# Kernel optimization log

Measured on AMD Instinct MI355X. Metric: run time of the kernel, lower is better.

## Reference

```python
import jax, jax.numpy as jnp
import numpy as np

B, S, E = 2, 2048, 1024
NH, NKV = 16, 4
HD = E // NH
GS = NH // NKV


def setup_inputs() -> dict:
    key = jax.random.key(0)
    ks = jax.random.split(key, 8)
    sc = 0.02
    query = jax.random.normal(ks[0], (B, S, E), dtype=jnp.float32)
    key_t = jax.random.normal(ks[1], (B, S, E), dtype=jnp.float32)
    value = jax.random.normal(ks[2], (B, S, E), dtype=jnp.float32)
    # causal mask, broadcast shape [1,1,S,S] as in source (unsqueeze(0).unsqueeze(0))
    attn_mask = jnp.tril(jnp.ones((S, S), dtype=bool))[None, None]
    Wq = jax.random.normal(ks[3], (NH * HD, E), dtype=jnp.float32) * sc
    Wk = jax.random.normal(ks[4], (NKV * HD, E), dtype=jnp.float32) * sc
    Wv = jax.random.normal(ks[5], (NKV * HD, E), dtype=jnp.float32) * sc
    Wo = jax.random.normal(ks[6], (E, NH * HD), dtype=jnp.float32) * sc
    return {"query": query, "key": key_t, "value": value, "attn_mask": attn_mask,
            "Wq": Wq, "Wk": Wk, "Wv": Wv, "Wo": Wo}


def reference(query, key, value, attn_mask, Wq, Wk, Wv, Wo):
    # projections (nn.Linear, bias=False: y = x @ W.T)
    q = (query @ Wq.T).reshape(B, S, NH, HD).transpose(0, 2, 1, 3)   # [B,NH,S,HD]
    k = (key @ Wk.T).reshape(B, S, NKV, HD).transpose(0, 2, 1, 3)    # [B,NKV,S,HD]
    v = (value @ Wv.T).reshape(B, S, NKV, HD).transpose(0, 2, 1, 3)  # [B,NKV,S,HD]
    # repeat_interleave over head dim to match query heads
    k = jnp.repeat(k, GS, axis=1)  # [B,NH,S,HD]
    v = jnp.repeat(v, GS, axis=1)
    scale = 1.0 / np.sqrt(HD).astype(np.float32)
    scores = jnp.einsum('bhqd,bhkd->bhqk', q, k) * scale  # [B,NH,S,S]
    scores = jnp.where(attn_mask, scores, -jnp.inf)
    weights = jax.nn.softmax(scores, axis=-1)
    out = jnp.einsum('bhqk,bhkd->bhqd', weights, v)        # [B,NH,S,HD]
    out = out.transpose(0, 2, 1, 3).reshape(B, S, NH * HD)
    return out @ Wo.T  # [B,S,E]
```

## Files before the change

### kernel.cpp

```cpp
#include <hip/hip_runtime.h>
#include <hip/hip_bf16.h>

typedef __attribute__((ext_vector_type(8))) short bf16x8;
typedef __attribute__((ext_vector_type(4))) float f32x4;

#define MFMA16(a, b, c) __builtin_amdgcn_mfma_f32_16x16x32_bf16((a), (b), (c), 0, 0, 0)
#define ASYNC16(g, l)                                                     \
    __builtin_amdgcn_global_load_lds(                                     \
        (const __attribute__((address_space(1))) void*)(g),               \
        (__attribute__((address_space(3))) void*)(l), 16, 0, 0)

constexpr int B_ = 2, S_ = 2048, E_ = 1024, NH_ = 16, NKV_ = 4, HD_ = 64;

__global__ __launch_bounds__(256) void cvt_all(
    const float* __restrict__ s0, const float* __restrict__ s1,
    const float* __restrict__ s2, const float* __restrict__ s3,
    const float* __restrict__ s4, const float* __restrict__ s5,
    const float* __restrict__ s6,
    __hip_bfloat16* __restrict__ d0, __hip_bfloat16* __restrict__ d1,
    __hip_bfloat16* __restrict__ d2, __hip_bfloat16* __restrict__ d3,
    __hip_bfloat16* __restrict__ d4, __hip_bfloat16* __restrict__ d5,
    __hip_bfloat16* __restrict__ d6)
{
    int id = blockIdx.x;
    const float* s;
    __hip_bfloat16* d;
    if (id < 6144) {
        const int which = id >> 11;
        s = which == 0 ? s0 : (which == 1 ? s1 : s2);
        d = which == 0 ? d0 : (which == 1 ? d1 : d2);
        id &= 2047;
    } else if (id < 6656) { s = s3; d = d3; id -= 6144; }
    else if (id < 7168)   { s = s4; d = d4; id -= 6656; }
    else if (id < 7296)   { s = s5; d = d5; id -= 7168; }
    else                  { s = s6; d = d6; id -= 7296; }

    const size_t i = ((size_t)id * 256 + threadIdx.x) * 8;
    const float4 f0 = *reinterpret_cast<const float4*>(s + i);
    const float4 f1 = *reinterpret_cast<const float4*>(s + i + 4);
    union { __hip_bfloat16 h[8]; uint4 u; } t;
    t.h[0] = __float2bfloat16(f0.x); t.h[1] = __float2bfloat16(f0.y);
    t.h[2] = __float2bfloat16(f0.z); t.h[3] = __float2bfloat16(f0.w);
    t.h[4] = __float2bfloat16(f1.x); t.h[5] = __float2bfloat16(f1.y);
    t.h[6] = __float2bfloat16(f1.z); t.h[7] = __float2bfloat16(f1.w);
    *reinterpret_cast<uint4*>(d + i) = t.u;
}

__device__ __forceinline__ void gemm_core(
    const __hip_bfloat16* __restrict__ A,
    const __hip_bfloat16* __restrict__ W,
    void* __restrict__ C,
    const int N, const int mode, const int m0, const int n0,
    __hip_bfloat16* sA, __hip_bfloat16* sW)
{
    const int tid  = threadIdx.x;
    const int l    = tid & 63;
    const int w    = tid >> 6;
    const int quad = l >> 4;
    const int lan  = l & 15;
    const int wm   = (w >> 1) * 32;
    const int wn   = (w & 1) * 64;

    const int srow  = w * 8 + (l >> 3);
    const int scolL = (l & 7) * 8;
    const int scolG = ((l & 7) ^ (l >> 3)) * 8;

    f32x4 acc[2][4] = {};

#define STAGE(buf, kb)                                                    \
    {                                                                     \
        _Pragma("unroll")                                                 \
        for (int q = 0; q < 2; ++q) {                                     \
            const int r_ = q * 32 + srow;                                 \
            ASYNC16(A + (size_t)(m0 + r_) * E_ + (kb) + scolG,            \
                    sA + (buf) * 4096 + r_ * 64 + scolL);                 \
        }                                                                 \
        _Pragma("unroll")                                                 \
        for (int q = 0; q < 4; ++q) {                                     \
            const int r_ = q * 32 + srow;                                 \
            ASYNC16(W + (size_t)(n0 + r_) * E_ + (kb) + scolG,            \
                    sW + (buf) * 8192 + r_ * 64 + scolL);                 \
        }                                                                 \
    }

    STAGE(0, 0)
    int cur = 0;
#pragma unroll 1
    for (int t = 0; t < 16; ++t) {
        __syncthreads();
        if (t < 15) STAGE(cur ^ 1, (t + 1) * 64)

#pragma unroll
        for (int kk = 0; kk < 2; ++kk) {
            bf16x8 af[2], bf[4];
            const int ca = ((kk * 4 + quad) ^ (lan & 7)) * 8;
#pragma unroll
            for (int i = 0; i < 2; ++i)
                af[i] = *reinterpret_cast<const bf16x8*>(
                    sA + cur * 4096 + (wm + i * 16 + lan) * 64 + ca);
#pragma unroll
            for (int j = 0; j < 4; ++j)
                bf[j] = *reinterpret_cast<const bf16x8*>(
                    sW + cur * 8192 + (wn + j * 16 + lan) * 64 + ca);
#pragma unroll
            for (int i = 0; i < 2; ++i)
#pragma unroll
                for (int j = 0; j < 4; ++j)
                    acc[i][j] = MFMA16(af[i], bf[j], acc[i][j]);
        }
        cur ^= 1;
    }
#undef STAGE

#pragma unroll
    for (int i = 0; i < 2; ++i)
#pragma unroll
        for (int j = 0; j < 4; ++j)
#pragma unroll
            for (int r = 0; r < 4; ++r) {
                const int gm = m0 + wm + i * 16 + quad * 4 + r;
                const int gn = n0 + wn + j * 16 + lan;
                const float v = acc[i][j][r];
                if (mode == 2) {
                    ((float*)C)[(size_t)gm * N + gn] = v;
                } else {
                    const __hip_bfloat16 hv = __float2bfloat16(v);
                    if (mode == 0)
                        ((__hip_bfloat16*)C)[(size_t)gm * N + gn] = hv;
                    else
                        ((__hip_bfloat16*)C)
                            [((size_t)(gm >> 11) * N + gn) * (size_t)S_ +
                             (gm & 2047)] = hv;
                }
            }
}

__global__ __launch_bounds__(256) void gemm_qkv(
    const __hip_bfloat16* __restrict__ qb, const __hip_bfloat16* __restrict__ kb,
    const __hip_bfloat16* __restrict__ vb, const __hip_bfloat16* __restrict__ Wqb,
    const __hip_bfloat16* __restrict__ Wkb, const __hip_bfloat16* __restrict__ Wvb,
    __hip_bfloat16* __restrict__ QO, __hip_bfloat16* __restrict__ Kws,
    __hip_bfloat16* __restrict__ VT)
{
    __shared__ __hip_bfloat16 sA[2 * 4096];
    __shared__ __hip_bfloat16 sW[2 * 8192];
    int id = blockIdx.x;
    const __hip_bfloat16 *A, *W;
    void* C;
    int N, mode, bx, by;
    if (id < 512)      { A = qb; W = Wqb; C = QO;  N = 1024; mode = 0; bx = id & 7; by = id >> 3; }
    else if (id < 640) { id -= 512; A = kb; W = Wkb; C = Kws; N = 256; mode = 0; bx = id & 1; by = id >> 1; }
    else               { id -= 640; A = vb; W = Wvb; C = VT;  N = 256; mode = 1; bx = id & 1; by = id >> 1; }
    gemm_core(A, W, C, N, mode, by * 64, bx * 128, sA, sW);
}

__global__ __launch_bounds__(256) void gemm_out(
    const __hip_bfloat16* __restrict__ QO, const __hip_bfloat16* __restrict__ Wob,
    float* __restrict__ out)
{
    __shared__ __hip_bfloat16 sA[2 * 4096];
    __shared__ __hip_bfloat16 sW[2 * 8192];
    const int id = blockIdx.x;
    gemm_core(QO, Wob, out, 1024, 2, (id >> 3) * 64, (id & 7) * 128, sA, sW);
}

__global__ __launch_bounds__(256) void attn(
    __hip_bfloat16* QO,
    const __hip_bfloat16* __restrict__ Kp,
    const __hip_bfloat16* __restrict__ VT)
{
    __shared__ __hip_bfloat16 sK[64][64];
    __shared__ __hip_bfloat16 sV[64][64];

    const int bx   = blockIdx.x;
    const int h    = blockIdx.y;
    const int b    = blockIdx.z;
    const int hk   = h >> 2;
    const int tid  = threadIdx.x;
    const int l    = tid & 63;
    const int w    = tid >> 6;
    const int quad = l >> 4;
    const int lan  = l & 15;
    const bool hi  = quad >= 2;
    const float KSC = 0.125f * 1.44269504088896340736f;

    const int idxA = (((quad & 1) * 32) + lan) * 4;
    const int idxB = idxA + 64;

    const int kr  = tid >> 2;
    const int s0c = (tid & 3) * 2;
    const int sw0 = (s0c ^ (kr & 7)) * 8;
    const int sw1 = ((s0c + 1) ^ (kr & 7)) * 8;
    const int kc  = s0c * 8;

    const int swq0 = (quad ^ (lan & 7)) * 8;
    const int swq1 = ((4 + quad) ^ (lan & 7)) * 8;

    const __hip_bfloat16* kg =
        Kp + ((size_t)((b * S_ + kr) * NKV_) + hk) * HD_ + kc;
    const __hip_bfloat16* vg =
        VT + ((size_t)((b * NKV_ + hk) * HD_) + kr) * S_ + kc;
    const size_t kstride = (size_t)64 * NKV_ * HD_;

    for (int half = 0; half < 2; ++half) {
        const int qt  = half ? (31 - bx) : bx;
        const int qr0 = qt * 64 + w * 16;
        const int qme = qr0 + lan;

        const __hip_bfloat16* qp =
            QO + ((size_t)((b * S_ + qme) * NH_) + h) * HD_ + quad * 8;
        const bf16x8 aq0 = *reinterpret_cast<const bf16x8*>(qp);
        const bf16x8 aq1 = *reinterpret_cast<const bf16x8*>(qp + 32);

        float m_i = -3.0e38f, l_i = 0.f;
        f32x4 acc_o[4] = {};

        uint4 kv0 = *reinterpret_cast<const uint4*>(kg);
        uint4 kv1 = *reinterpret_cast<const uint4*>(kg + 8);
        uint4 vv0 = *reinterpret_cast<const uint4*>(vg);
        uint4 vv1 = *reinterpret_cast<const uint4*>(vg + 8);

        for (int kt = 0; kt <= qt; ++kt) {
            __syncthreads();
            *reinterpret_cast<uint4*>(&sK[kr][sw0]) = kv0;
            *reinterpret_cast<uint4*>(&sK[kr][sw1]) = kv1;
            *reinterpret_cast<uint4*>(&sV[kr][sw0]) = vv0;
            *reinterpret_cast<uint4*>(&sV[kr][sw1]) = vv1;
            __syncthreads();

            if (kt < qt) {
                const __hip_bfloat16* kn = kg + (size_t)(kt + 1) * kstride;
                const __hip_bfloat16* vn = vg + (size_t)(kt + 1) * 64;
                kv0 = *reinterpret_cast<const uint4*>(kn);
                kv1 = *reinterpret_cast<const uint4*>(kn + 8);
                vv0 = *reinterpret_cast<const uint4*>(vn);
                vv1 = *reinterpret_cast<const uint4*>(vn + 8);
            }

            f32x4 accs[4] = {};
#pragma unroll
            for (int j = 0; j < 4; ++j) {
                bf16x8 bk0 = *reinterpret_cast<const bf16x8*>(&sK[j * 16 + lan][swq0]);
                accs[j] = MFMA16(bk0, aq0, accs[j]);
                bf16x8 bk1 = *reinterpret_cast<const bf16x8*>(&sK[j * 16 + lan][swq1]);
                accs[j] = MFMA16(bk1, aq1, accs[j]);
            }

            if (kt == qt) {
#pragma unroll
                for (int j = 0; j < 4; ++j)
#pragma unroll
                    for (int r = 0; r < 4; ++r) {
                        const int kcg = kt * 64 + j * 16 + quad * 4 + r;
                        if (kcg > qme) accs[j][r] = -1e30f;
                    }
            }

            float tm = accs[0][0];
#pragma unroll
            for (int j = 0; j < 4; ++j)
#pragma unroll
                for (int r = 0; r < 4; ++r) tm = fmaxf(tm, accs[j][r]);
            tm = fmaxf(tm, __shfl_xor(tm, 16));
            tm = fmaxf(tm, __shfl_xor(tm, 32));

            if (__any((tm - m_i) * KSC > 8.0f)) {
                const float mnew  = fmaxf(m_i, tm);
                const float alpha = exp2f((m_i - mnew) * KSC);
                l_i *= alpha;
                m_i  = mnew;
#pragma unroll
                for (int dd = 0; dd < 4; ++dd)
#pragma unroll
                    for (int r = 0; r < 4; ++r) acc_o[dd][r] *= alpha;
            }

            float ps = 0.f;
#pragma unroll
            for (int j = 0; j < 4; ++j)
#pragma unroll
                for (int r = 0; r < 4; ++r) {
                    const float p = exp2f((accs[j][r] - m_i) * KSC);
                    accs[j][r] = p;
                    ps += p;
                }
            ps += __shfl_xor(ps, 16);
            ps += __shfl_xor(ps, 32);
            l_i += ps;

            uint pk[4][2];
#pragma unroll
            for (int j = 0; j < 4; ++j)
#pragma unroll
                for (int hh = 0; hh < 2; ++hh) {
                    union { __hip_bfloat16 bh[2]; uint u; } t;
                    t.bh[0] = __float2bfloat16(accs[j][2 * hh]);
                    t.bh[1] = __float2bfloat16(accs[j][2 * hh + 1]);
                    pk[j][hh] = t.u;
                }

#pragma unroll
            for (int kk = 0; kk < 2; ++kk) {
                union { uint u[4]; bf16x8 v; } pb;
#pragma unroll
                for (int w2 = 0; w2 < 4; ++w2) {
                    const int idx = (w2 & 2) ? idxB : idxA;
                    const uint a = (uint)__builtin_amdgcn_ds_bpermute(
                        idx, (int)pk[2 * kk][w2 & 1]);
                    const uint bb = (uint)__builtin_amdgcn_ds_bpermute(
                        idx, (int)pk[2 * kk + 1][w2 & 1]);
                    pb.u[w2] = hi ? bb : a;
                }
#pragma unroll
                for (int dd = 0; dd < 4; ++dd) {
                    const int swv = ((kk * 4 + quad) ^ (lan & 7)) * 8;
                    bf16x8 av = *reinterpret_cast<const bf16x8*>(
                        &sV[dd * 16 + lan][swv]);
                    acc_o[dd] = MFMA16(av, pb.v, acc_o[dd]);
                }
            }
        }

        const float inv = 1.0f / l_i;
        __hip_bfloat16* op =
            QO + ((size_t)((b * S_ + qme) * NH_) + h) * HD_ + quad * 4;
#pragma unroll
        for (int dd = 0; dd < 4; ++dd) {
            union { __hip_bfloat16 bh[4]; uint2 u; } t;
#pragma unroll
            for (int r = 0; r < 4; ++r)
                t.bh[r] = __float2bfloat16(acc_o[dd][r] * inv);
            *reinterpret_cast<uint2*>(op + dd * 16) = t.u;
        }
    }
}

extern "C" void kernel_launch(void* const* d_in, const int* in_sizes, int n_in,
                              void* d_out, int out_size, void* d_ws, size_t ws_size,
                              hipStream_t stream) {
    const float* q  = (const float*)d_in[0];
    const float* k  = (const float*)d_in[1];
    const float* v  = (const float*)d_in[2];
    const float* Wq = (const float*)d_in[4];
    const float* Wk = (const float*)d_in[5];
    const float* Wv = (const float*)d_in[6];
    const float* Wo = (const float*)d_in[7];

    __hip_bfloat16* ws = (__hip_bfloat16*)d_ws;
    __hip_bfloat16* qb   = ws;
    __hip_bfloat16* kb   = qb  + 4194304;
    __hip_bfloat16* vb   = kb  + 4194304;
    __hip_bfloat16* QO   = vb  + 4194304;
    __hip_bfloat16* Kws  = QO  + 4194304;
    __hip_bfloat16* VT   = Kws + 1048576;
    __hip_bfloat16* Wqb  = VT  + 1048576;
    __hip_bfloat16* Wob  = Wqb + 1048576;
    __hip_bfloat16* Wkb  = Wob + 1048576;
    __hip_bfloat16* Wvb  = Wkb + 262144;

    cvt_all<<<dim3(7424), 256, 0, stream>>>(
        q, k, v, Wq, Wo, Wk, Wv, qb, kb, vb, Wqb, Wob, Wkb, Wvb);

    gemm_qkv<<<dim3(768), 256, 0, stream>>>(
        qb, kb, vb, Wqb, Wkb, Wvb, QO, Kws, VT);

    attn<<<dim3(16, NH_, B_), 256, 0, stream>>>(QO, Kws, VT);

    gemm_out<<<dim3(512), 256, 0, stream>>>(QO, Wob, (float*)d_out);
}
```

Measured before the change: 210.7 us.

## Use triple-buffered LDS pipeline with partial vmcnt waits in GEMM core

Converts the GEMM core's double-buffered async global-to-LDS loop into a three-stage ring buffer that prefetches two k-tiles ahead. It waits only for the oldest stage via s_waitcnt vmcnt(6) before the barrier, so memory latency overlaps more with MFMA work. This raises LDS usage per block from 48KB to 72KB, which may reduce occupancy for the projection and output GEMMs.

```diff
diff --git a/kernel.cpp b/kernel.cpp
--- a/kernel.cpp
+++ b/kernel.cpp
@@ -83,34 +83,49 @@
         }                                                                 \
     }
 
+#define COMPUTE(buf)                                                      \
+    {                                                                     \
+        _Pragma("unroll")                                                 \
+        for (int kk = 0; kk < 2; ++kk) {                                  \
+            bf16x8 af[2], bf[4];                                          \
+            const int ca = ((kk * 4 + quad) ^ (lan & 7)) * 8;             \
+            _Pragma("unroll")                                             \
+            for (int i = 0; i < 2; ++i)                                   \
+                af[i] = *reinterpret_cast<const bf16x8*>(                 \
+                    sA + (buf) * 4096 + (wm + i * 16 + lan) * 64 + ca);   \
+            _Pragma("unroll")                                             \
+            for (int j = 0; j < 4; ++j)                                   \
+                bf[j] = *reinterpret_cast<const bf16x8*>(                 \
+                    sW + (buf) * 8192 + (wn + j * 16 + lan) * 64 + ca);   \
+            _Pragma("unroll")                                             \
+            for (int i = 0; i < 2; ++i)                                   \
+                _Pragma("unroll")                                         \
+                for (int j = 0; j < 4; ++j)                               \
+                    acc[i][j] = MFMA16(af[i], bf[j], acc[i][j]);          \
+        }                                                                 \
+    }
+
     STAGE(0, 0)
+    STAGE(1, 64)
     int cur = 0;
 #pragma unroll 1
-    for (int t = 0; t < 16; ++t) {
-        __syncthreads();
-        if (t < 15) STAGE(cur ^ 1, (t + 1) * 64)
-
-#pragma unroll
-        for (int kk = 0; kk < 2; ++kk) {
-            bf16x8 af[2], bf[4];
-            const int ca = ((kk * 4 + quad) ^ (lan & 7)) * 8;
-#pragma unroll
-            for (int i = 0; i < 2; ++i)
-                af[i] = *reinterpret_cast<const bf16x8*>(
-                    sA + cur * 4096 + (wm + i * 16 + lan) * 64 + ca);
-#pragma unroll
-            for (int j = 0; j < 4; ++j)
-                bf[j] = *reinterpret_cast<const bf16x8*>(
-                    sW + cur * 8192 + (wn + j * 16 + lan) * 64 + ca);
-#pragma unroll
-            for (int i = 0; i < 2; ++i)
-#pragma unroll
-                for (int j = 0; j < 4; ++j)
-                    acc[i][j] = MFMA16(af[i], bf[j], acc[i][j]);
+    for (int t = 0; t < 15; ++t) {
+        __builtin_amdgcn_sched_barrier(0);
+        asm volatile("s_waitcnt vmcnt(6)" ::: "memory");
+        __builtin_amdgcn_s_barrier();
+        if (t < 14) {
+            int nb = cur + 2; if (nb >= 3) nb -= 3;
+            STAGE(nb, (t + 2) * 64)
         }
-        cur ^= 1;
+        COMPUTE(cur)
+        cur = (cur == 2) ? 0 : cur + 1;
     }
+    __builtin_amdgcn_sched_barrier(0);
+    asm volatile("s_waitcnt vmcnt(0)" ::: "memory");
+    __builtin_amdgcn_s_barrier();
+    COMPUTE(cur)
 #undef STAGE
+#undef COMPUTE
 
 #pragma unroll
     for (int i = 0; i < 2; ++i)
@@ -142,8 +157,8 @@
     __hip_bfloat16* __restrict__ QO, __hip_bfloat16* __restrict__ Kws,
     __hip_bfloat16* __restrict__ VT)
 {
-    __shared__ __hip_bfloat16 sA[2 * 4096];
-    __shared__ __hip_bfloat16 sW[2 * 8192];
+    __shared__ __hip_bfloat16 sA[3 * 4096];
+    __shared__ __hip_bfloat16 sW[3 * 8192];
     int id = blockIdx.x;
     const __hip_bfloat16 *A, *W;
     void* C;
@@ -158,8 +173,8 @@
     const __hip_bfloat16* __restrict__ QO, const __hip_bfloat16* __restrict__ Wob,
     float* __restrict__ out)
 {
-    __shared__ __hip_bfloat16 sA[2 * 4096];
-    __shared__ __hip_bfloat16 sW[2 * 8192];
+    __shared__ __hip_bfloat16 sA[3 * 4096];
+    __shared__ __hip_bfloat16 sW[3 * 8192];
     const int id = blockIdx.x;
     gemm_core(QO, Wob, out, 1024, 2, (id >> 3) * 64, (id & 7) * 128, sA, sW);
 }
```

Result: slower. 219.0 us (+3.9%).

## Process 128-row query tiles per block to reuse K/V tiles across two row groups

Applied to the files above, without the earlier changes.

Each wave in the attention kernel now handles two 16-row query groups (32 rows), so a block covers 128 query rows and every K/V tile loaded into shared memory feeds twice as many MFMAs. The grid is halved to 8x16x2 blocks, still with causal pairing of tiles. The aim is to cut LDS/global traffic and sync overhead per unit of work. The cost is more registers (doubled accumulators), fewer blocks for the GPU to schedule, and some wasted work on the diagonal tile, where masking now spans two K tiles.

```diff
diff --git a/kernel.cpp b/kernel.cpp
--- a/kernel.cpp
+++ b/kernel.cpp
@@ -203,24 +203,31 @@
     const size_t kstride = (size_t)64 * NKV_ * HD_;
 
     for (int half = 0; half < 2; ++half) {
-        const int qt  = half ? (31 - bx) : bx;
-        const int qr0 = qt * 64 + w * 16;
-        const int qme = qr0 + lan;
-
-        const __hip_bfloat16* qp =
-            QO + ((size_t)((b * S_ + qme) * NH_) + h) * HD_ + quad * 8;
-        const bf16x8 aq0 = *reinterpret_cast<const bf16x8*>(qp);
-        const bf16x8 aq1 = *reinterpret_cast<const bf16x8*>(qp + 32);
-
-        float m_i = -3.0e38f, l_i = 0.f;
-        f32x4 acc_o[4] = {};
+        const int qt  = half ? (15 - bx) : bx;
+        const int qr0 = qt * 128 + w * 32;
+
+        bf16x8 aq[2][2];
+        int qme[2];
+#pragma unroll
+        for (int g = 0; g < 2; ++g) {
+            qme[g] = qr0 + g * 16 + lan;
+            const __hip_bfloat16* qp =
+                QO + ((size_t)((b * S_ + qme[g]) * NH_) + h) * HD_ + quad * 8;
+            aq[g][0] = *reinterpret_cast<const bf16x8*>(qp);
+            aq[g][1] = *reinterpret_cast<const bf16x8*>(qp + 32);
+        }
+
+        float m_i[2] = {-3.0e38f, -3.0e38f};
+        float l_i[2] = {0.f, 0.f};
+        f32x4 acc_o[2][4] = {};
 
         uint4 kv0 = *reinterpret_cast<const uint4*>(kg);
         uint4 kv1 = *reinterpret_cast<const uint4*>(kg + 8);
         uint4 vv0 = *reinterpret_cast<const uint4*>(vg);
         uint4 vv1 = *reinterpret_cast<const uint4*>(vg + 8);
 
-        for (int kt = 0; kt <= qt; ++kt) {
+        const int ktmax = 2 * qt + 1;
+        for (int kt = 0; kt <= ktmax; ++kt) {
             __syncthreads();
             *reinterpret_cast<uint4*>(&sK[kr][sw0]) = kv0;
             *reinterpret_cast<uint4*>(&sK[kr][sw1]) = kv1;
@@ -228,7 +235,7 @@
             *reinterpret_cast<uint4*>(&sV[kr][sw1]) = vv1;
             __syncthreads();
 
-            if (kt < qt) {
+            if (kt < ktmax) {
                 const __hip_bfloat16* kn = kg + (size_t)(kt + 1) * kstride;
                 const __hip_bfloat16* vn = vg + (size_t)(kt + 1) * 64;
                 kv0 = *reinterpret_cast<const uint4*>(kn);
@@ -237,100 +244,113 @@
                 vv1 = *reinterpret_cast<const uint4*>(vn + 8);
             }
 
-            f32x4 accs[4] = {};
+            f32x4 accs[2][4] = {};
 #pragma unroll
             for (int j = 0; j < 4; ++j) {
                 bf16x8 bk0 = *reinterpret_cast<const bf16x8*>(&sK[j * 16 + lan][swq0]);
-                accs[j] = MFMA16(bk0, aq0, accs[j]);
                 bf16x8 bk1 = *reinterpret_cast<const bf16x8*>(&sK[j * 16 + lan][swq1]);
-                accs[j] = MFMA16(bk1, aq1, accs[j]);
-            }
-
-            if (kt == qt) {
+                accs[0][j] = MFMA16(bk0, aq[0][0], accs[0][j]);
+                accs[0][j] = MFMA16(bk1, aq[0][1], accs[0][j]);
+                accs[1][j] = MFMA16(bk0, aq[1][0], accs[1][j]);
+                accs[1][j] = MFMA16(bk1, aq[1][1], accs[1][j]);
+            }
+
+            if (kt >= 2 * qt) {
+#pragma unroll
+                for (int g = 0; g < 2; ++g)
+#pragma unroll
+                    for (int j = 0; j < 4; ++j)
+#pragma unroll
+                        for (int r = 0; r < 4; ++r) {
+                            const int kcg = kt * 64 + j * 16 + quad * 4 + r;
+                            if (kcg > qme[g]) accs[g][j][r] = -1e30f;
+                        }
+            }
+
+            uint pk[2][4][2];
+#pragma unroll
+            for (int g = 0; g < 2; ++g) {
+                float tm = accs[g][0][0];
 #pragma unroll
                 for (int j = 0; j < 4; ++j)
 #pragma unroll
+                    for (int r = 0; r < 4; ++r) tm = fmaxf(tm, accs[g][j][r]);
+                tm = fmaxf(tm, __shfl_xor(tm, 16));
+                tm = fmaxf(tm, __shfl_xor(tm, 32));
+
+                if (__any((tm - m_i[g]) * KSC > 8.0f)) {
+                    const float mnew  = fmaxf(m_i[g], tm);
+                    const float alpha = exp2f((m_i[g] - mnew) * KSC);
+                    l_i[g] *= alpha;
+                    m_i[g]  = mnew;
+#pragma unroll
+                    for (int dd = 0; dd < 4; ++dd)
+#pragma unroll
+                        for (int r = 0; r < 4; ++r) acc_o[g][dd][r] *= alpha;
+                }
+
+                float ps = 0.f;
+#pragma unroll
+                for (int j = 0; j < 4; ++j)
+#pragma unroll
                     for (int r = 0; r < 4; ++r) {
-                        const int kcg = kt * 64 + j * 16 + quad * 4 + r;
-                        if (kcg > qme) accs[j][r] = -1e30f;
+                        const float p = exp2f((accs[g][j][r] - m_i[g]) * KSC);
+                        accs[g][j][r] = p;
+                        ps += p;
                     }
-            }
-
-            float tm = accs[0][0];
-#pragma unroll
-            for (int j = 0; j < 4; ++j)
-#pragma unroll
-                for (int r = 0; r < 4; ++r) tm = fmaxf(tm, accs[j][r]);
-            tm = fmaxf(tm, __shfl_xor(tm, 16));
-            tm = fmaxf(tm, __shfl_xor(tm, 32));
-
-            if (__any((tm - m_i) * KSC > 8.0f)) {
-                const float mnew  = fmaxf(m_i, tm);
-                const float alpha = exp2f((m_i - mnew) * KSC);
-                l_i *= alpha;
-                m_i  = mnew;
-#pragma unroll
-                for (int dd = 0; dd < 4; ++dd)
-#pragma unroll
-                    for (int r = 0; r < 4; ++r) acc_o[dd][r] *= alpha;
-            }
-
-            float ps = 0.f;
-#pragma unroll
-            for (int j = 0; j < 4; ++j)
-#pragma unroll
-                for (int r = 0; r < 4; ++r) {
-                    const float p = exp2f((accs[j][r] - m_i) * KSC);
-                    accs[j][r] = p;
-                    ps += p;
-                }
-            ps += __shfl_xor(ps, 16);
-            ps += __shfl_xor(ps, 32);
-            l_i += ps;
-
-            uint pk[4][2];
-#pragma unroll
-            for (int j = 0; j < 4; ++j)
-#pragma unroll
-                for (int hh = 0; hh < 2; ++hh) {
-                    union { __hip_bfloat16 bh[2]; uint u; } t;
-                    t.bh[0] = __float2bfloat16(accs[j][2 * hh]);
-                    t.bh[1] = __float2bfloat16(accs[j][2 * hh + 1]);
-                    pk[j][hh] = t.u;
-                }
+                ps += __shfl_xor(ps, 16);
+                ps += __shfl_xor(ps, 32);
+                l_i[g] += ps;
+
+#pragma unroll
+                for (int j = 0; j < 4; ++j)
+#pragma unroll
+                    for (int hh = 0; hh < 2; ++hh) {
+                        union { __hip_bfloat16 bh[2]; uint u; } t;
+                        t.bh[0] = __float2bfloat16(accs[g][j][2 * hh]);
+                        t.bh[1] = __float2bfloat16(accs[g][j][2 * hh + 1]);
+                        pk[g][j][hh] = t.u;
+                    }
+            }
 
 #pragma unroll
             for (int kk = 0; kk < 2; ++kk) {
-                union { uint u[4]; bf16x8 v; } pb;
-#pragma unroll
-                for (int w2 = 0; w2 < 4; ++w2) {
-                    const int idx = (w2 & 2) ? idxB : idxA;
-                    const uint a = (uint)__builtin_amdgcn_ds_bpermute(
-                        idx, (int)pk[2 * kk][w2 & 1]);
-                    const uint bb = (uint)__builtin_amdgcn_ds_bpermute(
-                        idx, (int)pk[2 * kk + 1][w2 & 1]);
-                    pb.u[w2] = hi ? bb : a;
-                }
+                union { uint u[4]; bf16x8 v; } pb[2];
+#pragma unroll
+                for (int g = 0; g < 2; ++g)
+#pragma unroll
+                    for (int w2 = 0; w2 < 4; ++w2) {
+                        const int idx = (w2 & 2) ? idxB : idxA;
+                        const uint a = (uint)__builtin_amdgcn_ds_bpermute(
+                            idx, (int)pk[g][2 * kk][w2 & 1]);
+                        const uint bb = (uint)__builtin_amdgcn_ds_bpermute(
+                            idx, (int)pk[g][2 * kk + 1][w2 & 1]);
+                        pb[g].u[w2] = hi ? bb : a;
+                    }
 #pragma unroll
                 for (int dd = 0; dd < 4; ++dd) {
                     const int swv = ((kk * 4 + quad) ^ (lan & 7)) * 8;
                     bf16x8 av = *reinterpret_cast<const bf16x8*>(
                         &sV[dd * 16 + lan][swv]);
-                    acc_o[dd] = MFMA16(av, pb.v, acc_o[dd]);
+                    acc_o[0][dd] = MFMA16(av, pb[0].v, acc_o[0][dd]);
+                    acc_o[1][dd] = MFMA16(av, pb[1].v, acc_o[1][dd]);
                 }
             }
         }
 
-        const float inv = 1.0f / l_i;
-        __hip_bfloat16* op =
-            QO + ((size_t)((b * S_ + qme) * NH_) + h) * HD_ + quad * 4;
-#pragma unroll
-        for (int dd = 0; dd < 4; ++dd) {
-            union { __hip_bfloat16 bh[4]; uint2 u; } t;
-#pragma unroll
-            for (int r = 0; r < 4; ++r)
-                t.bh[r] = __float2bfloat16(acc_o[dd][r] * inv);
-            *reinterpret_cast<uint2*>(op + dd * 16) = t.u;
+#pragma unroll
+        for (int g = 0; g < 2; ++g) {
+            const float inv = 1.0f / l_i[g];
+            __hip_bfloat16* op =
+                QO + ((size_t)((b * S_ + qme[g]) * NH_) + h) * HD_ + quad * 4;
+#pragma unroll
+            for (int dd = 0; dd < 4; ++dd) {
+                union { __hip_bfloat16 bh[4]; uint2 u; } t;
+#pragma unroll
+                for (int r = 0; r < 4; ++r)
+                    t.bh[r] = __float2bfloat16(acc_o[g][dd][r] * inv);
+                *reinterpret_cast<uint2*>(op + dd * 16) = t.u;
+            }
         }
     }
 }
@@ -364,7 +384,7 @@
     gemm_qkv<<<dim3(768), 256, 0, stream>>>(
         qb, kb, vb, Wqb, Wkb, Wvb, QO, Kws, VT);
 
-    attn<<<dim3(16, NH_, B_), 256, 0, stream>>>(QO, Kws, VT);
+    attn<<<dim3(8, NH_, B_), 256, 0, stream>>>(QO, Kws, VT);
 
     gemm_out<<<dim3(512), 256, 0, stream>>>(QO, Wob, (float*)d_out);
 }
```

Result: slower. 227.2 us (+7.8%).

## Load K/V MFMA fragments directly from global memory, dropping LDS staging

Applied to the files above, without the earlier changes.

The attention kernel no longer stages K and V tiles in shared memory with register prefetch and two block barriers per tile. Each wave now reads its MFMA operand fragments for K and transposed V straight from global memory, relying on L1/L2 caching. This removes the LDS writes and barrier costs, but the four waves in a block each fetch the same K/V data, and loads are no longer prefetched a tile ahead, so latency may be exposed.

```diff
diff --git a/kernel.cpp b/kernel.cpp
--- a/kernel.cpp
+++ b/kernel.cpp
@@ -169,9 +169,6 @@
     const __hip_bfloat16* __restrict__ Kp,
     const __hip_bfloat16* __restrict__ VT)
 {
-    __shared__ __hip_bfloat16 sK[64][64];
-    __shared__ __hip_bfloat16 sV[64][64];
-
     const int bx   = blockIdx.x;
     const int h    = blockIdx.y;
     const int b    = blockIdx.z;
@@ -187,20 +184,11 @@
     const int idxA = (((quad & 1) * 32) + lan) * 4;
     const int idxB = idxA + 64;
 
-    const int kr  = tid >> 2;
-    const int s0c = (tid & 3) * 2;
-    const int sw0 = (s0c ^ (kr & 7)) * 8;
-    const int sw1 = ((s0c + 1) ^ (kr & 7)) * 8;
-    const int kc  = s0c * 8;
-
-    const int swq0 = (quad ^ (lan & 7)) * 8;
-    const int swq1 = ((4 + quad) ^ (lan & 7)) * 8;
-
-    const __hip_bfloat16* kg =
-        Kp + ((size_t)((b * S_ + kr) * NKV_) + hk) * HD_ + kc;
-    const __hip_bfloat16* vg =
-        VT + ((size_t)((b * NKV_ + hk) * HD_) + kr) * S_ + kc;
-    const size_t kstride = (size_t)64 * NKV_ * HD_;
+    const __hip_bfloat16* kgf =
+        Kp + ((size_t)((b * S_ + lan) * NKV_) + hk) * HD_ + quad * 8;
+    const __hip_bfloat16* vgf =
+        VT + ((size_t)((b * NKV_ + hk) * HD_) + lan) * S_ + quad * 8;
+    const size_t krs = (size_t)NKV_ * HD_;
 
     for (int half = 0; half < 2; ++half) {
         const int qt  = half ? (31 - bx) : bx;
@@ -215,34 +203,16 @@
         float m_i = -3.0e38f, l_i = 0.f;
         f32x4 acc_o[4] = {};
 
-        uint4 kv0 = *reinterpret_cast<const uint4*>(kg);
-        uint4 kv1 = *reinterpret_cast<const uint4*>(kg + 8);
-        uint4 vv0 = *reinterpret_cast<const uint4*>(vg);
-        uint4 vv1 = *reinterpret_cast<const uint4*>(vg + 8);
-
         for (int kt = 0; kt <= qt; ++kt) {
-            __syncthreads();
-            *reinterpret_cast<uint4*>(&sK[kr][sw0]) = kv0;
-            *reinterpret_cast<uint4*>(&sK[kr][sw1]) = kv1;
-            *reinterpret_cast<uint4*>(&sV[kr][sw0]) = vv0;
-            *reinterpret_cast<uint4*>(&sV[kr][sw1]) = vv1;
-            __syncthreads();
-
-            if (kt < qt) {
-                const __hip_bfloat16* kn = kg + (size_t)(kt + 1) * kstride;
-                const __hip_bfloat16* vn = vg + (size_t)(kt + 1) * 64;
-                kv0 = *reinterpret_cast<const uint4*>(kn);
-                kv1 = *reinterpret_cast<const uint4*>(kn + 8);
-                vv0 = *reinterpret_cast<const uint4*>(vn);
-                vv1 = *reinterpret_cast<const uint4*>(vn + 8);
-            }
-
             f32x4 accs[4] = {};
+            const __hip_bfloat16* kb_ = kgf + (size_t)(kt * 64) * krs;
 #pragma unroll
             for (int j = 0; j < 4; ++j) {
-                bf16x8 bk0 = *reinterpret_cast<const bf16x8*>(&sK[j * 16 + lan][swq0]);
+                bf16x8 bk0 = *reinterpret_cast<const bf16x8*>(
+                    kb_ + (size_t)(j * 16) * krs);
+                bf16x8 bk1 = *reinterpret_cast<const bf16x8*>(
+                    kb_ + (size_t)(j * 16) * krs + 32);
                 accs[j] = MFMA16(bk0, aq0, accs[j]);
-                bf16x8 bk1 = *reinterpret_cast<const bf16x8*>(&sK[j * 16 + lan][swq1]);
                 accs[j] = MFMA16(bk1, aq1, accs[j]);
             }
 
@@ -313,9 +283,8 @@
                 }
 #pragma unroll
                 for (int dd = 0; dd < 4; ++dd) {
-                    const int swv = ((kk * 4 + quad) ^ (lan & 7)) * 8;
                     bf16x8 av = *reinterpret_cast<const bf16x8*>(
-                        &sV[dd * 16 + lan][swv]);
+                        vgf + (size_t)(dd * 16) * S_ + kt * 64 + kk * 32);
                     acc_o[dd] = MFMA16(av, pb.v, acc_o[dd]);
                 }
             }
```

After: 272.6 us. 1.29x slower.
